# Optimization experiments

Hardware: AMD Instinct MI355X
Metric: run time of the kernel (lower is better)

The kernel has to match this reference:

```python
import jax, jax.numpy as jnp
import numpy as np
from math import factorial, sqrt

RS_IN = [(64, 0, 0), (64, 1, 0), (32, 2, 0)]
BATCH = 256


def _w3j(j1, j2, j3, m1, m2, m3):
    # Racah formula for the Wigner 3j symbol (integer l's)
    if m1 + m2 + m3 != 0 or not (abs(j1 - j2) <= j3 <= j1 + j2):
        return 0.0
    if abs(m1) > j1 or abs(m2) > j2 or abs(m3) > j3:
        return 0.0
    f = factorial
    pref = (-1.0) ** (j1 - j2 - m3) * sqrt(
        f(j1 + j2 - j3) * f(j1 - j2 + j3) * f(-j1 + j2 + j3) / f(j1 + j2 + j3 + 1)
        * f(j1 + m1) * f(j1 - m1) * f(j2 + m2) * f(j2 - m2) * f(j3 + m3) * f(j3 - m3))
    kmin = max(0, j2 - j3 - m1, j1 - j3 + m2)
    kmax = min(j1 + j2 - j3, j1 - m1, j2 + m2)
    s = 0.0
    for k in range(kmin, kmax + 1):
        s += (-1.0) ** k / (f(k) * f(j1 + j2 - j3 - k) * f(j1 - m1 - k)
                            * f(j2 + m2 - k) * f(j3 - j2 + m1 + k) * f(j3 - j1 - m2 + k))
    return pref * s


def _q(l):
    # unitary change of basis: complex spherical harmonics -> real basis
    q = np.zeros((2 * l + 1, 2 * l + 1), dtype=complex)
    q[l, l] = 1.0
    for m in range(1, l + 1):
        q[l + m, l + m] = (-1) ** m / sqrt(2)
        q[l + m, l - m] = 1 / sqrt(2)
        q[l - m, l - m] = 1j / sqrt(2)
        q[l - m, l + m] = -1j * (-1) ** m / sqrt(2)
    return q


def _real_w3j(la, lb, lc):
    # real-basis Wigner 3j tensor of shape (2la+1, 2lb+1, 2lc+1), Frobenius norm 1
    Cc = np.zeros((2 * la + 1, 2 * lb + 1, 2 * lc + 1))
    for ma in range(-la, la + 1):
        for mb in range(-lb, lb + 1):
            mc = -(ma + mb)
            if abs(mc) <= lc:
                Cc[la + ma, lb + mb, lc + mc] = _w3j(la, lb, lc, ma, mb, mc)
    T = np.einsum('im,jn,ko,mno->ijk', _q(la), _q(lb), _q(lc), Cc.astype(complex))
    idx = np.argmax(np.abs(T))
    T = T / (T.flat[idx] / abs(T.flat[idx]))  # fix global phase -> real tensor
    assert np.abs(T.imag).max() < 1e-6
    return np.real(T)


def _simplify(Rs):
    out = []
    for mul, l, p in Rs:
        if out and out[-1][1:] == (l, p):
            out[-1] = (out[-1][0] + mul, l, p)
        elif mul > 0:
            out.append((mul, l, p))
    return out


def _build(Rs_in):
    # Replicates e3nn tensor_square(Rs_in, sorted=True) with 'component' normalization,
    # producing the sparse mixing matrix as (row, col_i, col_j, value) with
    # col = col_i * dim_in + col_j  (never materialized densely).
    Rs = _simplify(Rs_in)
    dim_in = sum(m * (2 * l + 1) for m, l, _ in Rs)
    rows, ci, cj, vals, Rs_out = [], [], [], [], []
    index_out = 0
    index_1 = 0
    for a, (mul1, l1, p1) in enumerate(Rs):
        dim1 = mul1 * (2 * l1 + 1)
        # diagonal block: irrep with itself (sym/antisym multiplicity pairs)
        for lo in range(0, 2 * l1 + 1):
            w_all = np.arange(mul1 * mul1)
            u, v = w_all // mul1, w_all % mul1
            mask = (u <= v) if lo % 2 == 0 else (u < v)
            u, v = u[mask], v[mask]
            cnt = u.size
            if cnt == 0:
                continue
            C = _real_w3j(lo, l1, l1) * sqrt(2 * lo + 1)  # component norm
            k, i1, i2 = np.nonzero(C)
            cv = C[k, i1, i2]
            w = np.arange(cnt)
            rows.append((w[:, None] * (2 * lo + 1) + k[None, :]).ravel() + index_out)
            ci.append((u[:, None] * (2 * l1 + 1) + i1[None, :]).ravel() + index_1)
            cj.append((v[:, None] * (2 * l1 + 1) + i2[None, :]).ravel() + index_1)
            vals.append(np.tile(cv, cnt))
            Rs_out.append((cnt, lo, p1 * p1))
            index_out += cnt * (2 * lo + 1)
        index_2 = index_1 + dim1
        # off-diagonal blocks
        for (mul2, l2, p2) in Rs[a + 1:]:
            dim2 = mul2 * (2 * l2 + 1)
            for lo in range(abs(l1 - l2), l1 + l2 + 1):
                C = _real_w3j(lo, l1, l2) * sqrt(2 * lo + 1)
                k, i1, i2 = np.nonzero(C)
                cv = C[k, i1, i2]
                cnt = mul1 * mul2
                w = np.arange(cnt)
                u, v = w // mul2, w % mul2
                rows.append((w[:, None] * (2 * lo + 1) + k[None, :]).ravel() + index_out)
                ci.append((u[:, None] * (2 * l1 + 1) + i1[None, :]).ravel() + index_1)
                cj.append((v[:, None] * (2 * l2 + 1) + i2[None, :]).ravel() + index_2)
                vals.append(np.tile(cv, cnt))
                Rs_out.append((cnt, lo, p1 * p2))
                index_out += cnt * (2 * lo + 1)
            index_2 += dim2
        index_1 += dim1
    Rs_out = _simplify(Rs_out)
    # stable sort of output irreps by (l, p) -> row permutation (sorted=True)
    xs, j = [], 0
    for mul, l, p in Rs_out:
        d = mul * (2 * l + 1)
        xs.append((l, p, mul, j, d))
        j += d
    old2new = np.empty(j, dtype=np.int64)
    i = 0
    for l, p, mul, jj, d in sorted(xs):
        old2new[jj:jj + d] = np.arange(i, i + d)
        i += d
    rows = old2new[np.concatenate(rows)]
    return (rows.astype(np.int32), np.concatenate(ci).astype(np.int32),
            np.concatenate(cj).astype(np.int32),
            np.concatenate(vals).astype(np.float32), int(i), int(dim_in))


_ROWS, _COLI, _COLJ, _VALS, _DIM_OUT, _DIM_IN = _build(RS_IN)


def setup_inputs() -> dict:
    key = jax.random.key(0)
    features = jax.random.normal(key, (BATCH, _DIM_IN), dtype=jnp.float32)
    return {
        'features': features,
        'vals': jnp.asarray(_VALS),
        'rows': jnp.asarray(_ROWS),
        'col_i': jnp.asarray(_COLI),
        'col_j': jnp.asarray(_COLJ),
        'dim_out': _DIM_OUT,
    }


def reference(features, vals, rows, col_i, col_j, dim_out):
    # out[z, r] = sum_e vals[e] * f[z, col_i[e]] * f[z, col_j[e]]  scattered into rows[e]
    f = features.reshape(-1, features.shape[-1])              # (Z, dim_in)
    contrib = vals[None, :] * f[:, col_i] * f[:, col_j]       # (Z, nnz)
    out = jax.ops.segment_sum(contrib.T, rows, num_segments=dim_out)  # (dim_out, Z)
    return out.T.reshape(*features.shape[:-1], -1)
```

## Files before the change

### kernel.cpp

```cpp
#include <hip/hip_runtime.h>

#define BATCH 256
#define ZTILE 16
#define YSPLIT 3
#define PADF 20
#define DIN_CAP 416

__global__ __launch_bounds__(256) void prep_t(
    const float* __restrict__ f, const int* __restrict__ rows,
    int* __restrict__ rstart, int* __restrict__ rend,
    float* __restrict__ fT, int nnz, int dim_in, int TB, int ctiles)
{
    const int bx = blockIdx.x;
    if (bx < TB) {
        __shared__ float lt[32][33];
        const int c0 = (bx % ctiles) * 32;
        const int z0 = (bx / ctiles) * 32;
        const int ic = threadIdx.x & 31;
        const int i0 = threadIdx.x >> 5;
#pragma unroll
        for (int k = 0; k < 4; ++k) {
            const int a = i0 + 8 * k;
            const int c = c0 + ic;
            lt[a][ic] = (c < dim_in) ? f[(size_t)(z0 + a) * dim_in + c] : 0.0f;
        }
        __syncthreads();
#pragma unroll
        for (int k = 0; k < 4; ++k) {
            const int b = i0 + 8 * k;
            const int c = c0 + b;
            if (c < dim_in)
                fT[(size_t)c * BATCH + z0 + ic] = lt[ic][b];
        }
    } else {
        const int e = (bx - TB) * 256 + threadIdx.x;
        if (e < nnz) {
            const int r = rows[e];
            if (e == 0 || rows[e - 1] != r) rstart[r] = e;
            if (e == nnz - 1 || rows[e + 1] != r) rend[r] = e + 1;
        }
    }
}

__device__ __forceinline__ void lds_sync()
{
    asm volatile("s_waitcnt lgkmcnt(0)" ::: "memory");
    __builtin_amdgcn_sched_barrier(0);
    __builtin_amdgcn_s_barrier();
    __builtin_amdgcn_sched_barrier(0);
}

__global__ __launch_bounds__(256) void tsq_main(
    const float* __restrict__ fT, const float* __restrict__ vals,
    const int* __restrict__ ci, const int* __restrict__ cj,
    const int* __restrict__ rstart, const int* __restrict__ rend,
    float* __restrict__ out, int dim_in, int dim_out, int nnz)
{
    __shared__ __align__(16) float fzT[DIN_CAP * PADF];

    const int r = blockIdx.x * 256 + threadIdx.x;
    const bool valid = (r < dim_out);

    int s = 0, e1 = 0;
    if (valid) {
        const int ss = rstart[r];
        const int ee = rend[r];
        if (ss >= 0 && ee > ss && ee <= nnz) { s = ss; e1 = ee; }
    }

    const int nchunk = dim_in * (ZTILE / 4);
    const int ntile  = BATCH / ZTILE;

    for (int t = blockIdx.y; t < ntile; t += YSPLIT) {
        const int z0 = t * ZTILE;

        for (int i = threadIdx.x; i < nchunk; i += 256) {
            const int c  = i >> 2;
            const int zq = i & 3;
            const float4 v = *(const float4*)(fT + (size_t)c * BATCH + z0 + zq * 4);
            *(float4*)(fzT + c * PADF + zq * 4) = v;
        }
        lds_sync();

        float4 a0 = {0,0,0,0}, a1 = {0,0,0,0}, a2 = {0,0,0,0}, a3 = {0,0,0,0};
        for (int e = s; e < e1; ++e) {
            const int   a = ci[e];
            const int   b = cj[e];
            const float v = vals[e];
            const float* ba = fzT + a * PADF;
            const float* bb = fzT + b * PADF;
            float4 xa, xb;
            xa = *(const float4*)(ba);      xb = *(const float4*)(bb);
            a0.x += v*xa.x*xb.x; a0.y += v*xa.y*xb.y; a0.z += v*xa.z*xb.z; a0.w += v*xa.w*xb.w;
            xa = *(const float4*)(ba + 4);  xb = *(const float4*)(bb + 4);
            a1.x += v*xa.x*xb.x; a1.y += v*xa.y*xb.y; a1.z += v*xa.z*xb.z; a1.w += v*xa.w*xb.w;
            xa = *(const float4*)(ba + 8);  xb = *(const float4*)(bb + 8);
            a2.x += v*xa.x*xb.x; a2.y += v*xa.y*xb.y; a2.z += v*xa.z*xb.z; a2.w += v*xa.w*xb.w;
            xa = *(const float4*)(ba + 12); xb = *(const float4*)(bb + 12);
            a3.x += v*xa.x*xb.x; a3.y += v*xa.y*xb.y; a3.z += v*xa.z*xb.z; a3.w += v*xa.w*xb.w;
        }

        if (valid) {
            float* o = out + (size_t)z0 * dim_out + r;
            const size_t d = dim_out;
            o[0]      = a0.x;  o[d]      = a0.y;  o[2*d]  = a0.z;  o[3*d]  = a0.w;
            o[4*d]    = a1.x;  o[5*d]    = a1.y;  o[6*d]  = a1.z;  o[7*d]  = a1.w;
            o[8*d]    = a2.x;  o[9*d]    = a2.y;  o[10*d] = a2.z;  o[11*d] = a2.w;
            o[12*d]   = a3.x;  o[13*d]   = a3.y;  o[14*d] = a3.z;  o[15*d] = a3.w;
        }
        lds_sync();
    }
}

__global__ __launch_bounds__(256) void tsq_fallback(
    const float* __restrict__ f, const float* __restrict__ vals,
    const int* __restrict__ ci, const int* __restrict__ cj,
    const int* __restrict__ rstart, const int* __restrict__ rend,
    float* __restrict__ out, int dim_in, int dim_out, int nnz)
{
    const int r = blockIdx.x * blockDim.x + threadIdx.x;
    if (r >= dim_out) return;
    const int z = blockIdx.y;
    const float* __restrict__ fb = f + (size_t)z * dim_in;
    const int ss = rstart[r];
    const int ee = rend[r];
    float acc = 0.0f;
    if (ss >= 0 && ee > ss && ee <= nnz) {
        for (int e = ss; e < ee; ++e)
            acc += vals[e] * fb[ci[e]] * fb[cj[e]];
    }
    out[(size_t)z * dim_out + r] = acc;
}

extern "C" void kernel_launch(void* const* d_in, const int* in_sizes, int n_in,
                              void* d_out, int out_size, void* d_ws, size_t ws_size,
                              hipStream_t stream)
{
    const float* f    = (const float*)d_in[0];
    const float* vals = (const float*)d_in[1];
    const int*   rows = (const int*)d_in[2];
    const int*   ci   = (const int*)d_in[3];
    const int*   cj   = (const int*)d_in[4];
    float*       out  = (float*)d_out;

    const int nnz     = in_sizes[1];
    const int nF      = in_sizes[0];
    const int dim_in  = nF / BATCH;
    const int dim_out = out_size / BATCH;

    int*   rstart = (int*)d_ws;
    int*   rend   = rstart + dim_out;
    float* fT     = (float*)(rend + dim_out);

    const int use_main = (dim_in <= DIN_CAP) &&
                         (ws_size >= (size_t)(2 * dim_out) * 4 + (size_t)nF * 4);

    const int ctiles = (dim_in + 31) / 32;
    const int TB = use_main ? ctiles * (BATCH / 32) : 0;
    const int NB = (nnz + 255) / 256;
    prep_t<<<TB + NB, 256, 0, stream>>>(f, rows, rstart, rend, fT,
                                        nnz, dim_in, TB, ctiles);

    if (use_main) {
        dim3 grid((dim_out + 255) / 256, YSPLIT);
        tsq_main<<<grid, 256, 0, stream>>>(fT, vals, ci, cj, rstart, rend, out,
                                           dim_in, dim_out, nnz);
    } else {
        dim3 grid((dim_out + 255) / 256, BATCH);
        tsq_fallback<<<grid, 256, 0, stream>>>(f, vals, ci, cj, rstart, rend,
                                               out, dim_in, dim_out, nnz);
    }
}
```

Measured before the change: 36.81 us.

## Fuse prep and main kernels into one cooperative kernel with grid sync

Replaces the two-launch sequence (transpose plus row-range kernel, then the main contraction) with a single cooperative kernel. It does the prep work, calls a grid-wide sync, then processes the (row-block, z-tile) work items in a grid-stride loop, which spreads work across more blocks than the previous YSPLIT=3 grid. This is meant to remove a kernel launch gap and raise parallelism. In exchange it adds grid-sync overhead and a host-side occupancy query on every call, and the generic fallback kernel is removed.

```diff
diff --git a/kernel.cpp b/kernel.cpp
--- a/kernel.cpp
+++ b/kernel.cpp
@@ -1,10 +1,124 @@
 #include <hip/hip_runtime.h>
+#include <hip/hip_cooperative_groups.h>
+
+namespace cg = cooperative_groups;
 
 #define BATCH 256
 #define ZTILE 16
 #define YSPLIT 3
 #define PADF 20
 #define DIN_CAP 416
+
+__device__ __forceinline__ void lds_sync()
+{
+    asm volatile("s_waitcnt lgkmcnt(0)" ::: "memory");
+    __builtin_amdgcn_sched_barrier(0);
+    __builtin_amdgcn_s_barrier();
+    __builtin_amdgcn_sched_barrier(0);
+}
+
+__global__ __launch_bounds__(256) void tsq_fused(
+    const float* __restrict__ f, const float* __restrict__ vals,
+    const int* __restrict__ ci, const int* __restrict__ cj,
+    const int* __restrict__ rows, int* __restrict__ rstart,
+    int* __restrict__ rend, float* __restrict__ fT,
+    float* __restrict__ out,
+    int nnz, int dim_in, int dim_out, int TB, int ctiles, int nxblk)
+{
+    __shared__ __align__(16) char smem[DIN_CAP * PADF * 4];
+
+    const int tid = threadIdx.x;
+    const int b   = blockIdx.x;
+    const int G   = gridDim.x;
+
+    {
+        float (*lt)[33] = (float (*)[33])smem;
+        for (int w = b; w < TB; w += G) {
+            const int c0 = (w % ctiles) * 32;
+            const int z0 = (w / ctiles) * 32;
+            const int ic = tid & 31;
+            const int i0 = tid >> 5;
+#pragma unroll
+            for (int k = 0; k < 4; ++k) {
+                const int a = i0 + 8 * k;
+                const int c = c0 + ic;
+                lt[a][ic] = (c < dim_in) ? f[(size_t)(z0 + a) * dim_in + c] : 0.0f;
+            }
+            __syncthreads();
+#pragma unroll
+            for (int k = 0; k < 4; ++k) {
+                const int bb = i0 + 8 * k;
+                const int c  = c0 + bb;
+                if (c < dim_in)
+                    fT[(size_t)c * BATCH + z0 + ic] = lt[ic][bb];
+            }
+            __syncthreads();
+        }
+    }
+    for (int e = b * 256 + tid; e < nnz; e += G * 256) {
+        const int rr = rows[e];
+        if (e == 0 || rows[e - 1] != rr) rstart[rr] = e;
+        if (e == nnz - 1 || rows[e + 1] != rr) rend[rr] = e + 1;
+    }
+
+    cg::this_grid().sync();
+
+    float* fzT = (float*)smem;
+    const int nchunk = dim_in * (ZTILE / 4);
+    const int ntile  = BATCH / ZTILE;
+    const int nwork  = nxblk * ntile;
+
+    for (int w = b; w < nwork; w += G) {
+        const int xb = w % nxblk;
+        const int t  = w / nxblk;
+        const int z0 = t * ZTILE;
+        const int r  = xb * 256 + tid;
+        const bool valid = (r < dim_out);
+
+        int s = 0, e1 = 0;
+        if (valid) {
+            const int ss = rstart[r];
+            const int ee = rend[r];
+            if (ss >= 0 && ee > ss && ee <= nnz) { s = ss; e1 = ee; }
+        }
+
+        for (int i = tid; i < nchunk; i += 256) {
+            const int c  = i >> 2;
+            const int zq = i & 3;
+            const float4 v = *(const float4*)(fT + (size_t)c * BATCH + z0 + zq * 4);
+            *(float4*)(fzT + c * PADF + zq * 4) = v;
+        }
+        lds_sync();
+
+        float4 a0 = {0,0,0,0}, a1 = {0,0,0,0}, a2 = {0,0,0,0}, a3 = {0,0,0,0};
+        for (int e = s; e < e1; ++e) {
+            const int   a  = ci[e];
+            const int   bb = cj[e];
+            const float v  = vals[e];
+            const float* ba = fzT + a * PADF;
+            const float* bc = fzT + bb * PADF;
+            float4 xa, xb;
+            xa = *(const float4*)(ba);      xb = *(const float4*)(bc);
+            a0.x += v*xa.x*xb.x; a0.y += v*xa.y*xb.y; a0.z += v*xa.z*xb.z; a0.w += v*xa.w*xb.w;
+            xa = *(const float4*)(ba + 4);  xb = *(const float4*)(bc + 4);
+            a1.x += v*xa.x*xb.x; a1.y += v*xa.y*xb.y; a1.z += v*xa.z*xb.z; a1.w += v*xa.w*xb.w;
+            xa = *(const float4*)(ba + 8);  xb = *(const float4*)(bc + 8);
+            a2.x += v*xa.x*xb.x; a2.y += v*xa.y*xb.y; a2.z += v*xa.z*xb.z; a2.w += v*xa.w*xb.w;
+            xa = *(const float4*)(ba + 12); xb = *(const float4*)(bc + 12);
+            a3.x += v*xa.x*xb.x; a3.y += v*xa.y*xb.y; a3.z += v*xa.z*xb.z; a3.w += v*xa.w*xb.w;
+        }
+
+        if (valid) {
+            float* o = out + (size_t)z0 * dim_out + r;
+            const size_t d = dim_out;
+            o[0]    = a0.x;  o[d]    = a0.y;  o[2*d]  = a0.z;  o[3*d]  = a0.w;
+            o[4*d]  = a1.x;  o[5*d]  = a1.y;  o[6*d]  = a1.z;  o[7*d]  = a1.w;
+            o[8*d]  = a2.x;  o[9*d]  = a2.y;  o[10*d] = a2.z;  o[11*d] = a2.w;
+            o[12*d] = a3.x;  o[13*d] = a3.y;  o[14*d] = a3.z;  o[15*d] = a3.w;
+        }
+        lds_sync();
+    }
+}
 
 __global__ __launch_bounds__(256) void prep_t(
     const float* __restrict__ f, const int* __restrict__ rows,
@@ -27,10 +141,10 @@
         __syncthreads();
 #pragma unroll
         for (int k = 0; k < 4; ++k) {
-            const int b = i0 + 8 * k;
-            const int c = c0 + b;
+            const int bb = i0 + 8 * k;
+            const int c  = c0 + bb;
             if (c < dim_in)
-                fT[(size_t)c * BATCH + z0 + ic] = lt[ic][b];
+                fT[(size_t)c * BATCH + z0 + ic] = lt[ic][bb];
         }
     } else {
         const int e = (bx - TB) * 256 + threadIdx.x;
@@ -42,14 +156,6 @@
     }
 }
 
-__device__ __forceinline__ void lds_sync()
-{
-    asm volatile("s_waitcnt lgkmcnt(0)" ::: "memory");
-    __builtin_amdgcn_sched_barrier(0);
-    __builtin_amdgcn_s_barrier();
-    __builtin_amdgcn_sched_barrier(0);
-}
-
 __global__ __launch_bounds__(256) void tsq_main(
     const float* __restrict__ fT, const float* __restrict__ vals,
     const int* __restrict__ ci, const int* __restrict__ cj,
@@ -69,11 +175,8 @@
     }
 
     const int nchunk = dim_in * (ZTILE / 4);
-    const int ntile  = BATCH / ZTILE;
-
-    for (int t = blockIdx.y; t < ntile; t += YSPLIT) {
+    for (int t = blockIdx.y; t < BATCH / ZTILE; t += YSPLIT) {
         const int z0 = t * ZTILE;
-
         for (int i = threadIdx.x; i < nchunk; i += 256) {
             const int c  = i >> 2;
             const int zq = i & 3;
@@ -84,52 +187,32 @@
 
         float4 a0 = {0,0,0,0}, a1 = {0,0,0,0}, a2 = {0,0,0,0}, a3 = {0,0,0,0};
         for (int e = s; e < e1; ++e) {
-            const int   a = ci[e];
-            const int   b = cj[e];
-            const float v = vals[e];
+            const int   a  = ci[e];
+            const int   bb = cj[e];
+            const float v  = vals[e];
             const float* ba = fzT + a * PADF;
-            const float* bb = fzT + b * PADF;
+            const float* bc = fzT + bb * PADF;
             float4 xa, xb;
-            xa = *(const float4*)(ba);      xb = *(const float4*)(bb);
+            xa = *(const float4*)(ba);      xb = *(const float4*)(bc);
             a0.x += v*xa.x*xb.x; a0.y += v*xa.y*xb.y; a0.z += v*xa.z*xb.z; a0.w += v*xa.w*xb.w;
-            xa = *(const float4*)(ba + 4);  xb = *(const float4*)(bb + 4);
+            xa = *(const float4*)(ba + 4);  xb = *(const float4*)(bc + 4);
             a1.x += v*xa.x*xb.x; a1.y += v*xa.y*xb.y; a1.z += v*xa.z*xb.z; a1.w += v*xa.w*xb.w;
-            xa = *(const float4*)(ba + 8);  xb = *(const float4*)(bb + 8);
+            xa = *(const float4*)(ba + 8);  xb = *(const float4*)(bc + 8);
             a2.x += v*xa.x*xb.x; a2.y += v*xa.y*xb.y; a2.z += v*xa.z*xb.z; a2.w += v*xa.w*xb.w;
-            xa = *(const float4*)(ba + 12); xb = *(const float4*)(bb + 12);
+            xa = *(const float4*)(ba + 12); xb = *(const float4*)(bc + 12);
             a3.x += v*xa.x*xb.x; a3.y += v*xa.y*xb.y; a3.z += v*xa.z*xb.z; a3.w += v*xa.w*xb.w;
         }
 
         if (valid) {
             float* o = out + (size_t)z0 * dim_out + r;
             const size_t d = dim_out;
-            o[0]      = a0.x;  o[d]      = a0.y;  o[2*d]  = a0.z;  o[3*d]  = a0.w;
-            o[4*d]    = a1.x;  o[5*d]    = a1.y;  o[6*d]  = a1.z;  o[7*d]  = a1.w;
-            o[8*d]    = a2.x;  o[9*d]    = a2.y;  o[10*d] = a2.z;  o[11*d] = a2.w;
-            o[12*d]   = a3.x;  o[13*d]   = a3.y;  o[14*d] = a3.z;  o[15*d] = a3.w;
-        }
-        lds_sync();
-    }
-}
-
-__global__ __launch_bounds__(256) void tsq_fallback(
-    const float* __restrict__ f, const float* __restrict__ vals,
-    const int* __restrict__ ci, const int* __restrict__ cj,
-    const int* __restrict__ rstart, const int* __restrict__ rend,
-    float* __restrict__ out, int dim_in, int dim_out, int nnz)
-{
-    const int r = blockIdx.x * blockDim.x + threadIdx.x;
-    if (r >= dim_out) return;
-    const int z = blockIdx.y;
-    const float* __restrict__ fb = f + (size_t)z * dim_in;
-    const int ss = rstart[r];
-    const int ee = rend[r];
-    float acc = 0.0f;
-    if (ss >= 0 && ee > ss && ee <= nnz) {
-        for (int e = ss; e < ee; ++e)
-            acc += vals[e] * fb[ci[e]] * fb[cj[e]];
-    }
-    out[(size_t)z * dim_out + r] = acc;
+            o[0]    = a0.x;  o[d]    = a0.y;  o[2*d]  = a0.z;  o[3*d]  = a0.w;
+            o[4*d]  = a1.x;  o[5*d]  = a1.y;  o[6*d]  = a1.z;  o[7*d]  = a1.w;
+            o[8*d]  = a2.x;  o[9*d]  = a2.y;  o[10*d] = a2.z;  o[11*d] = a2.w;
+            o[12*d] = a3.x;  o[13*d] = a3.y;  o[14*d] = a3.z;  o[15*d] = a3.w;
+        }
+        lds_sync();
+    }
 }
 
 extern "C" void kernel_launch(void* const* d_in, const int* in_sizes, int n_in,
@@ -152,22 +235,40 @@
     int*   rend   = rstart + dim_out;
     float* fT     = (float*)(rend + dim_out);
 
-    const int use_main = (dim_in <= DIN_CAP) &&
-                         (ws_size >= (size_t)(2 * dim_out) * 4 + (size_t)nF * 4);
-
     const int ctiles = (dim_in + 31) / 32;
-    const int TB = use_main ? ctiles * (BATCH / 32) : 0;
-    const int NB = (nnz + 255) / 256;
-    prep_t<<<TB + NB, 256, 0, stream>>>(f, rows, rstart, rend, fT,
-                                        nnz, dim_in, TB, ctiles);
-
-    if (use_main) {
-        dim3 grid((dim_out + 255) / 256, YSPLIT);
+    const int TB     = ctiles * (BATCH / 32);
+    const int nxblk  = (dim_out + 255) / 256;
+
+    const bool ws_ok = (dim_in <= DIN_CAP) &&
+        (ws_size >= (size_t)(2 * dim_out) * 4 + (size_t)nF * 4);
+
+    bool launched = false;
+    if (ws_ok) {
+        int maxb = 0;
+        hipError_t oe = hipOccupancyMaxActiveBlocksPerMultiprocessor(
+            &maxb, tsq_fused, 256, 0);
+        int numCU = 0;
+        hipDeviceGetAttribute(&numCU, hipDeviceAttributeMultiprocessorCount, 0);
+        if (oe == hipSuccess && maxb > 0 && numCU > 0) {
+            int G = maxb * numCU;
+            const int nwork = nxblk * (BATCH / ZTILE);
+            if (G > nwork) G = nwork;
+            void* args[] = {
+                (void*)&f, (void*)&vals, (void*)&ci, (void*)&cj, (void*)&rows,
+                (void*)&rstart, (void*)&rend, (void*)&fT, (void*)&out,
+                (void*)&nnz, (void*)&dim_in, (void*)&dim_out,
+                (void*)&TB, (void*)&ctiles, (void*)&nxblk };
+            launched = (hipLaunchCooperativeKernel((const void*)tsq_fused,
+                        dim3(G), dim3(256), args, 0, stream) == hipSuccess);
+        }
+    }
+
+    if (!launched && ws_ok) {
+        const int NB = (nnz + 255) / 256;
+        prep_t<<<TB + NB, 256, 0, stream>>>(f, rows, rstart, rend, fT,
+                                            nnz, dim_in, TB, ctiles);
+        dim3 grid(nxblk, YSPLIT);
         tsq_main<<<grid, 256, 0, stream>>>(fT, vals, ci, cj, rstart, rend, out,
                                            dim_in, dim_out, nnz);
-    } else {
-        dim3 grid((dim_out + 255) / 256, BATCH);
-        tsq_fallback<<<grid, 256, 0, stream>>>(f, vals, ci, cj, rstart, rend,
-                                               out, dim_in, dim_out, nnz);
-    }
-}
+    }
+}
```

Measured after the change: 108.9 us. +195.8%, slower.
